# Optimization experiments

Hardware: AMD Instinct MI355X
Metric: run time of the kernel (lower is better)

Reference implementation:

```python
import jax, jax.numpy as jnp
from jax import lax
import numpy as np

# Problem dims (from init_kwargs / input_specs)
B, NC, NX, NY = 16, 31, 256, 256   # cube: batch, spectral channels, spatial
NO, KX, KY = 3, 17, 17             # diffraction orders, kernel spatial size
PAD = 4                            # findclusters dilation padding
N_LOC = NO * NC * (2 * PAD + 1) ** 2  # 7533 trainable kernel entries


def _build_locations():
    """Emulate findclusters: one dispersion delta per (order, channel),
    dilated by a (2*PAD+1)^2 window. Returns flat int32 indices into
    the flattened (NO, NC, KX, KY) kernel."""
    idxs = []
    cy = KX // 2  # 8
    lo, hi = PAD, KX - 1 - PAD  # valid center range [4, 12]
    for o in range(NO):
        for c in range(NC):
            # channel-dependent horizontal dispersion, order-dependent sign
            shift = (o - 1) * (c * PAD * 2 // (NC - 1))
            cx = int(np.clip(cy + shift, lo, hi))
            for dy in range(-PAD, PAD + 1):
                for dx in range(-PAD, PAD + 1):
                    idxs.append(((o * NC + c) * KX + (cy + dy)) * KY + (cx + dx))
    return jnp.asarray(np.array(idxs, dtype=np.int32))


def setup_inputs() -> dict:
    key = jax.random.key(0)
    k1, k2 = jax.random.split(key)
    x = jax.random.normal(k1, (B, NC, NX, NY), dtype=jnp.float32)
    # trainable sparse kernel values (mostly positive so ReLU passes most)
    variable_kernel = jax.random.uniform(k2, (N_LOC,), dtype=jnp.float32,
                                         minval=-0.2, maxval=1.0)
    locations = _build_locations()
    return {"x": x, "variable_kernel": variable_kernel, "locations": locations}


def reference(x, variable_kernel, locations):
    # fill_kernel: scatter ReLU'd trainable values into a zero kernel
    kernel = (jnp.zeros((NO * NC * KX * KY,), x.dtype)
              .at[locations].set(jax.nn.relu(variable_kernel))
              .reshape(NO, NC, KX, KY))
    # disperse_all_orders: per-order dispersion conv, summed over spectral
    # channels -> measurement per order. out: (B, NO, NX, NY)
    out = lax.conv_general_dilated(
        x, kernel, window_strides=(1, 1), padding="SAME",
        dimension_numbers=("NCHW", "OIHW", "NCHW"))
    return out
```

## Files before the change

kernel.cpp:

```cpp
#include <hip/hip_runtime.h>

namespace {

constexpr int kB  = 16;
constexpr int kNC = 31;
constexpr int kNX = 256;
constexpr int kNY = 256;
constexpr int kNO = 3;
constexpr int kKS = 17;
constexpr int NOC = kNO * kNC;

constexpr int TX = 64;
constexpr int TY = 32;
constexpr int HTY = TY + 8;
constexpr int XP  = 85;
constexpr int WROW = 12;

__global__ void prep(const float* __restrict__ vk, const int* __restrict__ loc,
                     float* __restrict__ wrel, int* __restrict__ soTab)
{
    int i = blockIdx.x * 256 + threadIdx.x;
    if (i < NOC * 9 * WROW) {
        int row = i / WROW;
        int dx  = i - row * WROW;
        float v = 0.0f;
        if (dx < 9) {
            float t = vk[row * 9 + dx];
            v = t > 0.0f ? t : 0.0f;
        }
        wrel[i] = v;
    }
    if (i < NOC) {
        int cx = loc[i * 81] - (i * kKS + 4) * kKS + 4;
        soTab[i] = cx - 4;
    }
}

__global__ __launch_bounds__(256, 6)
void disperse_conv(const float* __restrict__ x,
                   const float* __restrict__ wrel,
                   const int* __restrict__ soTab,
                   float* __restrict__ out)
{
    __shared__ float xtile[HTY * XP];

    const int tid = threadIdx.x;
    const int x0 = blockIdx.x * TX;
    const int y0 = blockIdx.y * TY;
    const int bz = blockIdx.z;
    const int b  = bz / 3;
    const int o  = bz - 3 * b;

    const int tx = tid & 7;
    const int ty = tid >> 3;
    const int xo = tx * 8;

    float acc[8];
    #pragma unroll
    for (int j = 0; j < 8; ++j) acc[j] = 0.0f;

    for (int c = 0; c < kNC; ++c) {
        __syncthreads();
        const float* xc = x + (size_t)(b * kNC + c) * kNX * kNY;
        #pragma unroll
        for (int it = 0; it < 4; ++it) {
            int i = it * 256 + tid;
            if (i < HTY * 20) {
                int r = i / 20;
                int k = i - r * 20;
                int gy = y0 - 4 + r;
                int gx = x0 - 8 + k * 4;
                float4 v = make_float4(0.f, 0.f, 0.f, 0.f);
                if ((unsigned)gy < (unsigned)kNX && (unsigned)gx < (unsigned)kNY)
                    v = *(const float4*)(xc + (size_t)gy * kNY + gx);
                float* d = &xtile[r * XP + k * 4];
                d[0] = v.x; d[1] = v.y; d[2] = v.z; d[3] = v.w;
            }
        }
        __syncthreads();

        const int so = soTab[o * kNC + c];
        const float* wch = wrel + (size_t)((o * kNC + c) * 9) * WROW;

        #pragma unroll 1
        for (int dy = 0; dy < 9; ++dy) {
            const float* xt = &xtile[(ty + dy) * XP + xo + so];
            float xr[16];
            #pragma unroll
            for (int i = 0; i < 16; ++i) xr[i] = xt[i];

            const float4 wa = *(const float4*)(wch + dy * WROW);
            const float4 wb = *(const float4*)(wch + dy * WROW + 4);
            const float  w8 = wch[dy * WROW + 8];

            #pragma unroll
            for (int j = 0; j < 8; ++j) acc[j] = fmaf(wa.x, xr[j + 0], acc[j]);
            #pragma unroll
            for (int j = 0; j < 8; ++j) acc[j] = fmaf(wa.y, xr[j + 1], acc[j]);
            #pragma unroll
            for (int j = 0; j < 8; ++j) acc[j] = fmaf(wa.z, xr[j + 2], acc[j]);
            #pragma unroll
            for (int j = 0; j < 8; ++j) acc[j] = fmaf(wa.w, xr[j + 3], acc[j]);
            #pragma unroll
            for (int j = 0; j < 8; ++j) acc[j] = fmaf(wb.x, xr[j + 4], acc[j]);
            #pragma unroll
            for (int j = 0; j < 8; ++j) acc[j] = fmaf(wb.y, xr[j + 5], acc[j]);
            #pragma unroll
            for (int j = 0; j < 8; ++j) acc[j] = fmaf(wb.z, xr[j + 6], acc[j]);
            #pragma unroll
            for (int j = 0; j < 8; ++j) acc[j] = fmaf(wb.w, xr[j + 7], acc[j]);
            #pragma unroll
            for (int j = 0; j < 8; ++j) acc[j] = fmaf(w8,   xr[j + 8], acc[j]);
        }
    }

    size_t base = (((size_t)b * kNO + o) * kNX + (size_t)(y0 + ty)) * kNY
                  + (size_t)(x0 + xo);
    *(float4*)(out + base)     = make_float4(acc[0], acc[1], acc[2], acc[3]);
    *(float4*)(out + base + 4) = make_float4(acc[4], acc[5], acc[6], acc[7]);
}

}

extern "C" void kernel_launch(void* const* d_in, const int* in_sizes, int n_in,
                              void* d_out, int out_size, void* d_ws, size_t ws_size,
                              hipStream_t stream)
{
    const float* x  = (const float*)d_in[0];
    const float* vk = (const float*)d_in[1];
    const int* loc  = (const int*)d_in[2];
    float* outp = (float*)d_out;

    float* wrel = (float*)d_ws;
    int*   soTab = (int*)(wrel + NOC * 9 * WROW);

    dim3 pgrid((NOC * 9 * WROW + 255) / 256);
    hipLaunchKernelGGL(prep, pgrid, dim3(256), 0, stream, vk, loc, wrel, soTab);

    dim3 grid(kNY / TX, kNX / TY, kB * kNO);
    hipLaunchKernelGGL(disperse_conv, grid, dim3(256), 0, stream,
                       x, wrel, soTab, outp);
}
```

Measured before the change: 479.6 us.

## Use 4x4 register tiles with row reuse and aligned shifted weights

Each thread now computes a 4x4 output block instead of 1x8. Every shared-memory row it loads is reused across up to four output rows. The dispersion shift is split into an aligned part, applied at tile load time so shared-memory reads become aligned float4 loads, and a residual shift of 0-3, folded into 12-wide zero-padded weights. This cuts LDS traffic per FMA but adds zero-weight FMAs (12 instead of 9 taps), and the taller 64-row tile plus lower occupancy (3 blocks/SM) risks less latency hiding.

```diff
diff --git a/kernel.cpp b/kernel.cpp
--- a/kernel.cpp
+++ b/kernel.cpp
@@ -11,38 +11,42 @@
 constexpr int NOC = kNO * kNC;
 
 constexpr int TX = 64;
-constexpr int TY = 32;
+constexpr int TY = 64;
 constexpr int HTY = TY + 8;
-constexpr int XP  = 85;
-constexpr int WROW = 12;
+constexpr int TCOL = 76;
+constexpr int XP   = 80;
+constexpr int W12  = 12;
 
 __global__ void prep(const float* __restrict__ vk, const int* __restrict__ loc,
-                     float* __restrict__ wrel, int* __restrict__ soTab)
+                     float* __restrict__ w12, int* __restrict__ soaTab)
 {
     int i = blockIdx.x * 256 + threadIdx.x;
-    if (i < NOC * 9 * WROW) {
-        int row = i / WROW;
-        int dx  = i - row * WROW;
+    if (i < NOC * 9 * W12) {
+        int row = i / W12;
+        int dp  = i - row * W12;
+        int oc  = row / 9;
+        int so = loc[oc * 81] - (oc * kKS + 4) * kKS;
+        int rs = so & 3;
         float v = 0.0f;
-        if (dx < 9) {
-            float t = vk[row * 9 + dx];
+        if (dp >= rs && dp < rs + 9) {
+            float t = vk[row * 9 + (dp - rs)];
             v = t > 0.0f ? t : 0.0f;
         }
-        wrel[i] = v;
+        w12[i] = v;
     }
     if (i < NOC) {
-        int cx = loc[i * 81] - (i * kKS + 4) * kKS + 4;
-        soTab[i] = cx - 4;
+        int so = loc[i * 81] - (i * kKS + 4) * kKS;
+        soaTab[i] = so & ~3;
     }
 }
 
-__global__ __launch_bounds__(256, 6)
+__global__ __launch_bounds__(256, 3)
 void disperse_conv(const float* __restrict__ x,
-                   const float* __restrict__ wrel,
-                   const int* __restrict__ soTab,
+                   const float* __restrict__ w12,
+                   const int* __restrict__ soaTab,
                    float* __restrict__ out)
 {
-    __shared__ float xtile[HTY * XP];
+    __shared__ __align__(16) float xtile[HTY * XP];
 
     const int tid = threadIdx.x;
     const int x0 = blockIdx.x * TX;
@@ -51,73 +55,89 @@
     const int b  = bz / 3;
     const int o  = bz - 3 * b;
 
-    const int tx = tid & 7;
-    const int ty = tid >> 3;
-    const int xo = tx * 8;
+    const int tx = tid & 15;
+    const int ty = tid >> 4;
+    const int xo = tx * 4;
 
-    float acc[8];
+    float acc[4][4];
     #pragma unroll
-    for (int j = 0; j < 8; ++j) acc[j] = 0.0f;
+    for (int jr = 0; jr < 4; ++jr)
+        #pragma unroll
+        for (int jj = 0; jj < 4; ++jj)
+            acc[jr][jj] = 0.0f;
 
     for (int c = 0; c < kNC; ++c) {
+        const int soa = soaTab[o * kNC + c];
+        const float* wch = w12 + (size_t)((o * kNC + c) * 9) * W12;
+        const float* xc  = x + (size_t)(b * kNC + c) * kNX * kNY;
+
         __syncthreads();
-        const float* xc = x + (size_t)(b * kNC + c) * kNX * kNY;
         #pragma unroll
-        for (int it = 0; it < 4; ++it) {
+        for (int it = 0; it < 6; ++it) {
             int i = it * 256 + tid;
-            if (i < HTY * 20) {
-                int r = i / 20;
-                int k = i - r * 20;
+            if (i < HTY * 19) {
+                int r  = i / 19;
+                int mc = i - r * 19;
                 int gy = y0 - 4 + r;
-                int gx = x0 - 8 + k * 4;
+                int gx = x0 + soa - 8 + mc * 4;
                 float4 v = make_float4(0.f, 0.f, 0.f, 0.f);
                 if ((unsigned)gy < (unsigned)kNX && (unsigned)gx < (unsigned)kNY)
                     v = *(const float4*)(xc + (size_t)gy * kNY + gx);
-                float* d = &xtile[r * XP + k * 4];
-                d[0] = v.x; d[1] = v.y; d[2] = v.z; d[3] = v.w;
+                *(float4*)&xtile[r * XP + mc * 4] = v;
             }
         }
         __syncthreads();
 
-        const int so = soTab[o * kNC + c];
-        const float* wch = wrel + (size_t)((o * kNC + c) * 9) * WROW;
-
-        #pragma unroll 1
-        for (int dy = 0; dy < 9; ++dy) {
-            const float* xt = &xtile[(ty + dy) * XP + xo + so];
-            float xr[16];
-            #pragma unroll
-            for (int i = 0; i < 16; ++i) xr[i] = xt[i];
-
-            const float4 wa = *(const float4*)(wch + dy * WROW);
-            const float4 wb = *(const float4*)(wch + dy * WROW + 4);
-            const float  w8 = wch[dy * WROW + 8];
+        #pragma unroll
+        for (int m = 0; m < 12; ++m) {
+            const int row = ty * 4 + m;
+            const float* p = &xtile[row * XP + xo];
+            const float4 q0 = *(const float4*)(p);
+            const float4 q1 = *(const float4*)(p + 4);
+            const float4 q2 = *(const float4*)(p + 8);
+            const float4 q3 = *(const float4*)(p + 12);
+            const float xr[16] = { q0.x, q0.y, q0.z, q0.w,
+                                   q1.x, q1.y, q1.z, q1.w,
+                                   q2.x, q2.y, q2.z, q2.w,
+                                   q3.x, q3.y, q3.z, q3.w };
 
             #pragma unroll
-            for (int j = 0; j < 8; ++j) acc[j] = fmaf(wa.x, xr[j + 0], acc[j]);
-            #pragma unroll
-            for (int j = 0; j < 8; ++j) acc[j] = fmaf(wa.y, xr[j + 1], acc[j]);
-            #pragma unroll
-            for (int j = 0; j < 8; ++j) acc[j] = fmaf(wa.z, xr[j + 2], acc[j]);
-            #pragma unroll
-            for (int j = 0; j < 8; ++j) acc[j] = fmaf(wa.w, xr[j + 3], acc[j]);
-            #pragma unroll
-            for (int j = 0; j < 8; ++j) acc[j] = fmaf(wb.x, xr[j + 4], acc[j]);
-            #pragma unroll
-            for (int j = 0; j < 8; ++j) acc[j] = fmaf(wb.y, xr[j + 5], acc[j]);
-            #pragma unroll
-            for (int j = 0; j < 8; ++j) acc[j] = fmaf(wb.z, xr[j + 6], acc[j]);
-            #pragma unroll
-            for (int j = 0; j < 8; ++j) acc[j] = fmaf(wb.w, xr[j + 7], acc[j]);
-            #pragma unroll
-            for (int j = 0; j < 8; ++j) acc[j] = fmaf(w8,   xr[j + 8], acc[j]);
+            for (int jr = 0; jr < 4; ++jr) {
+                const int dy = m - jr;
+                if (dy < 0 || dy >= 9) continue;
+                const float* wr = wch + dy * W12;
+                const float4 wa = *(const float4*)(wr);
+                const float4 wb = *(const float4*)(wr + 4);
+                const float4 wc = *(const float4*)(wr + 8);
+
+                #pragma unroll
+                for (int jj = 0; jj < 4; ++jj) {
+                    float a = acc[jr][jj];
+                    a = fmaf(wa.x, xr[jj + 0], a);
+                    a = fmaf(wa.y, xr[jj + 1], a);
+                    a = fmaf(wa.z, xr[jj + 2], a);
+                    a = fmaf(wa.w, xr[jj + 3], a);
+                    a = fmaf(wb.x, xr[jj + 4], a);
+                    a = fmaf(wb.y, xr[jj + 5], a);
+                    a = fmaf(wb.z, xr[jj + 6], a);
+                    a = fmaf(wb.w, xr[jj + 7], a);
+                    a = fmaf(wc.x, xr[jj + 8], a);
+                    a = fmaf(wc.y, xr[jj + 9], a);
+                    a = fmaf(wc.z, xr[jj + 10], a);
+                    a = fmaf(wc.w, xr[jj + 11], a);
+                    acc[jr][jj] = a;
+                }
+            }
         }
     }
 
-    size_t base = (((size_t)b * kNO + o) * kNX + (size_t)(y0 + ty)) * kNY
-                  + (size_t)(x0 + xo);
-    *(float4*)(out + base)     = make_float4(acc[0], acc[1], acc[2], acc[3]);
-    *(float4*)(out + base + 4) = make_float4(acc[4], acc[5], acc[6], acc[7]);
+    #pragma unroll
+    for (int jr = 0; jr < 4; ++jr) {
+        size_t base = (((size_t)b * kNO + o) * kNX + (size_t)(y0 + ty * 4 + jr)) * kNY
+                      + (size_t)(x0 + xo);
+        *(float4*)(out + base) = make_float4(acc[jr][0], acc[jr][1],
+                                             acc[jr][2], acc[jr][3]);
+    }
 }
 
 }
@@ -131,13 +151,13 @@
     const int* loc  = (const int*)d_in[2];
     float* outp = (float*)d_out;
 
-    float* wrel = (float*)d_ws;
-    int*   soTab = (int*)(wrel + NOC * 9 * WROW);
+    float* w12 = (float*)d_ws;
+    int*   soaTab = (int*)(w12 + NOC * 9 * W12);
 
-    dim3 pgrid((NOC * 9 * WROW + 255) / 256);
-    hipLaunchKernelGGL(prep, pgrid, dim3(256), 0, stream, vk, loc, wrel, soTab);
+    dim3 pgrid((NOC * 9 * W12 + 255) / 256);
+    hipLaunchKernelGGL(prep, pgrid, dim3(256), 0, stream, vk, loc, w12, soaTab);
 
     dim3 grid(kNY / TX, kNX / TY, kB * kNO);
     hipLaunchKernelGGL(disperse_conv, grid, dim3(256), 0, stream,
-                       x, wrel, soTab, outp);
+                       x, w12, soaTab, outp);
 }
```

New measurement: 447.9 us. -6.6%, faster.
